# Performance work log

Hardware: AMD Instinct MI355X
Metric: run time of the kernel (lower is better)

## Reference

```python
import jax, jax.numpy as jnp
import numpy as np

# ---- constants from SystemsOfSprings.f ----
TS = 0.05                      # integration step h
K_G, C_G = 1.0, 2.0            # ground spring / damper (k1..k4, c1..c4)
K_I, C_I = 1.0, 0.0            # inter-agent spring / damper (k5..k10, c5..c10)
_L9 = float(np.sqrt(4.0 ** 2 + 1.5 ** 2))
EDGE_I = jnp.array([0, 1, 2, 3, 2, 3])          # springs 5,6,7,8,9,10
EDGE_J = jnp.array([1, 2, 3, 0, 0, 1])
EDGE_L = jnp.array([4.0, 1.5, 4.0, 1.5, _L9, _L9], dtype=jnp.float32)
XBAR = jnp.array([2.0, 2.0, 0.0, 0.0, -2.0, 2.0, 0.0, 0.0,
                  -2.0, -2.0, 0.0, 0.0, 2.0, -2.0, 0.0, 0.0], dtype=jnp.float32)


def _step(x, u, xbar):
    # x: (16,) = [px,py,vx,vy] x 4 agents; u: (8,) = 2 force inputs per agent
    px, py, vx, vy = x[0::4], x[1::4], x[2::4], x[3::4]      # (4,) each (Mx/My/Mvx/Mvy selections)
    xt, yt = xbar[0::4], xbar[1::4]

    # ground spring + damper forces (toward target, opposing velocity)
    dxt, dyt = px - xt, py - yt
    ang_t = jnp.arctan2(dyt, dxt)
    ang_v = jnp.arctan2(vy, vx)
    Fk0 = K_G * jnp.sqrt(dxt ** 2 + dyt ** 2)
    Fc0 = C_G * jnp.sqrt(vx ** 2 + vy ** 2)
    Fgx = -Fk0 * jnp.cos(ang_t) - Fc0 * jnp.cos(ang_v)
    Fgy = -Fk0 * jnp.sin(ang_t) - Fc0 * jnp.sin(ang_v)

    # inter-agent springs/dampers on the 6 edges (edge list, no 4x4 diagonal NaNs)
    dxe = px[EDGE_I] - px[EDGE_J]
    dye = py[EDGE_I] - py[EDGE_J]
    dvxe = vx[EDGE_I] - vx[EDGE_J]
    dvye = vy[EDGE_I] - vy[EDGE_J]
    Fke = K_I * (jnp.sqrt(dxe ** 2 + dye ** 2) - EDGE_L)
    Fce = C_I * jnp.sqrt(dvxe ** 2 + dvye ** 2)
    ang = jnp.arctan2(dye, dxe)      # angle from j toward i's perspective at i
    angv = jnp.arctan2(dvye, dvxe)
    cxe, sye = jnp.cos(ang), jnp.sin(ang)
    cve, sve = jnp.cos(angv), jnp.sin(angv)
    # force on agent i: -F*proj(i,j); on agent j: -F*proj(j,i) = +F*proj(i,j)
    z4 = jnp.zeros(4, x.dtype)
    Fsx = z4.at[EDGE_I].add(-Fke * cxe).at[EDGE_J].add(Fke * cxe)
    Fsy = z4.at[EDGE_I].add(-Fke * sye).at[EDGE_J].add(Fke * sye)
    Fdx = z4.at[EDGE_I].add(-Fce * cve).at[EDGE_J].add(Fce * cve)
    Fdy = z4.at[EDGE_I].add(-Fce * sve).at[EDGE_J].add(Fce * sve)

    accx = Fsx + Fdx + Fgx  # masses m1..m4 = 1
    accy = Fsy + Fdy + Fgy

    dx = jnp.zeros(16, x.dtype)
    dx = dx.at[0::4].set(vx).at[1::4].set(vy).at[2::4].set(accx).at[3::4].set(accy)
    Bu = jnp.zeros(16, x.dtype).at[2::4].set(u[0::2]).at[3::4].set(u[1::2])
    return x + (dx + Bu) * TS


def setup_inputs() -> dict:
    key = jax.random.key(0)
    kx, ku = jax.random.split(key)
    B = 1048576
    x = jax.random.normal(kx, (B, 16), dtype=jnp.float32)
    u = jax.random.normal(ku, (B, 8), dtype=jnp.float32)
    return {"t": 0, "x": x, "u": u, "w": jnp.zeros((16,), jnp.float32), "xbar": XBAR}


def reference(t, x, u, w, xbar):
    # t and w are unused, exactly as in the torch forward; batch via vmap
    return jax.vmap(lambda xi, ui: _step(xi, ui, xbar))(x, u)
```

## Files before the change

### kernel.cpp

```cpp
#include <hip/hip_runtime.h>
#include <math.h>


#define TS 0.05f

__global__ __launch_bounds__(256) void springs_node_kernel(
    const float* __restrict__ x,
    const float* __restrict__ u,
    float* __restrict__ out,
    int N)
{
    int g = blockIdx.x * blockDim.x + threadIdx.x;
    if (g >= N) return;

    int node = g & 3;

    float4 s  = reinterpret_cast<const float4*>(x)[g];
    float2 uc = reinterpret_cast<const float2*>(u)[g];

    float px = s.x, py = s.y, vx = s.z, vy = s.w;

    float xt = (node == 1 || node == 2) ? -2.f : 2.f;
    float yt = (node >= 2) ? -2.f : 2.f;

    float ax = -(px - xt) - 2.f * vx;
    float ay = -(py - yt) - 2.f * vy;

    const float Ld[3] = { 4.0f, 4.2720018727f , 1.5f };

#pragma unroll
    for (int d = 1; d <= 3; ++d) {
        float qx = __shfl_xor(px, d, 64);
        float qy = __shfl_xor(py, d, 64);
        float dx = px - qx;
        float dy = py - qy;
        float d2 = dx * dx + dy * dy;
        float L  = Ld[d - 1];

        float r    = sqrtf(d2);
        bool  nz   = (d2 > 0.f);
        float invr = nz ? (1.f / r) : 0.f;
        float c    = nz ? (dx * invr) : 1.f;
        float sn   = dy * invr;
        float Fk   = r - L;

        ax -= Fk * c;
        ay -= Fk * sn;
    }

    float4 r4;
    r4.x = px + TS * vx;
    r4.y = py + TS * vy;
    r4.z = vx + TS * (ax + uc.x);
    r4.w = vy + TS * (ay + uc.y);

    reinterpret_cast<float4*>(out)[g] = r4;
}

extern "C" void kernel_launch(void* const* d_in, const int* in_sizes, int n_in,
                              void* d_out, int out_size, void* d_ws, size_t ws_size,
                              hipStream_t stream) {
    const float* x = (const float*)d_in[1];
    const float* u = (const float*)d_in[2];
    float* out = (float*)d_out;

    int N = in_sizes[1] / 4;
    int block = 256;
    int grid = (N + block - 1) / block;
    springs_node_kernel<<<grid, block, 0, stream>>>(x, u, out, N);
}
```

Before: 147.0 us.

## Process two agent pairs per thread with DPP exchange and nontemporal stores

```diff
diff --git a/kernel.cpp b/kernel.cpp
--- a/kernel.cpp
+++ b/kernel.cpp
@@ -3,58 +3,107 @@
 
 
 #define TS 0.05f
+#define L9 4.2720018727f
 
-__global__ __launch_bounds__(256) void springs_node_kernel(
+typedef float f4v __attribute__((ext_vector_type(4)));
+
+__device__ __forceinline__ float dpp_xor1(float v) {
+    return __int_as_float(__builtin_amdgcn_update_dpp(
+        0, __float_as_int(v), 0xB1, 0xF, 0xF, true));
+}
+
+__device__ __forceinline__ void edge_acc(float dx, float dy, float L,
+                                         float& ax, float& ay) {
+    float d2   = dx * dx + dy * dy;
+    bool  nz   = d2 > 0.f;
+    float invr = nz ? rsqrtf(d2) : 0.f;
+    float r    = d2 * invr;
+    float c    = nz ? dx * invr : 1.f;
+    float sn   = dy * invr;
+    float Fk   = r - L;
+    ax -= Fk * c;
+    ay -= Fk * sn;
+}
+
+__device__ __forceinline__ void do_pair(int parity,
+                                        float4 a, float4 b, float4 uc,
+                                        float4& ra, float4& rb) {
+    float xtA = parity ? -2.f : 2.f;
+    float ytA = xtA;
+    float xtB = -xtA;
+    float ytB = ytA;
+
+    float axA = -(a.x - xtA) - 2.f * a.z;
+    float ayA = -(a.y - ytA) - 2.f * a.w;
+    float axB = -(b.x - xtB) - 2.f * b.z;
+    float ayB = -(b.y - ytB) - 2.f * b.w;
+
+    {
+        float dx = a.x - b.x, dy = a.y - b.y;
+        float d2   = dx * dx + dy * dy;
+        bool  nz   = d2 > 0.f;
+        float invr = nz ? rsqrtf(d2) : 0.f;
+        float r    = d2 * invr;
+        float c    = nz ? dx * invr : 1.f;
+        float sn   = dy * invr;
+        float Fk   = r - 4.0f;
+        float fx = Fk * c, fy = Fk * sn;
+        axA -= fx; ayA -= fy;
+        axB += fx; ayB += fy;
+    }
+
+    float pxA2 = dpp_xor1(a.x), pyA2 = dpp_xor1(a.y);
+    float pxB2 = dpp_xor1(b.x), pyB2 = dpp_xor1(b.y);
+
+    edge_acc(a.x - pxA2, a.y - pyA2, L9,   axA, ayA);
+    edge_acc(a.x - pxB2, a.y - pyB2, 1.5f, axA, ayA);
+    edge_acc(b.x - pxB2, b.y - pyB2, L9,   axB, ayB);
+    edge_acc(b.x - pxA2, b.y - pyA2, 1.5f, axB, ayB);
+
+    ra.x = a.x + TS * a.z;
+    ra.y = a.y + TS * a.w;
+    ra.z = a.z + TS * (axA + uc.x);
+    ra.w = a.w + TS * (ayA + uc.y);
+    rb.x = b.x + TS * b.z;
+    rb.y = b.y + TS * b.w;
+    rb.z = b.z + TS * (axB + uc.z);
+    rb.w = b.w + TS * (ayB + uc.w);
+}
+
+__device__ __forceinline__ void nt_store4(float4 v, float4* p) {
+    f4v t = { v.x, v.y, v.z, v.w };
+    __builtin_nontemporal_store(t, reinterpret_cast<f4v*>(p));
+}
+
+__global__ __launch_bounds__(256) void springs_pair2_kernel(
     const float* __restrict__ x,
     const float* __restrict__ u,
     float* __restrict__ out,
-    int N)
+    int T)
 {
     int g = blockIdx.x * blockDim.x + threadIdx.x;
-    if (g >= N) return;
+    if (g >= T) return;
+    int h = g + T;
 
-    int node = g & 3;
+    const float4* x4 = reinterpret_cast<const float4*>(x);
+    const float4* u4 = reinterpret_cast<const float4*>(u);
+    float4*       o4 = reinterpret_cast<float4*>(out);
 
-    float4 s  = reinterpret_cast<const float4*>(x)[g];
-    float2 uc = reinterpret_cast<const float2*>(u)[g];
+    float4 a0 = x4[2 * g];
+    float4 b0 = x4[2 * g + 1];
+    float4 a1 = x4[2 * h];
+    float4 b1 = x4[2 * h + 1];
+    float4 u0 = u4[g];
+    float4 u1 = u4[h];
 
-    float px = s.x, py = s.y, vx = s.z, vy = s.w;
+    float4 ra0, rb0, ra1, rb1;
+    do_pair(g & 1, a0, b0, u0, ra0, rb0);
+    do_pair(h & 1, a1, b1, u1, ra1, rb1);
 
-    float xt = (node == 1 || node == 2) ? -2.f : 2.f;
-    float yt = (node >= 2) ? -2.f : 2.f;
-
-    float ax = -(px - xt) - 2.f * vx;
-    float ay = -(py - yt) - 2.f * vy;
-
-    const float Ld[3] = { 4.0f, 4.2720018727f , 1.5f };
-
-#pragma unroll
-    for (int d = 1; d <= 3; ++d) {
-        float qx = __shfl_xor(px, d, 64);
-        float qy = __shfl_xor(py, d, 64);
-        float dx = px - qx;
-        float dy = py - qy;
-        float d2 = dx * dx + dy * dy;
-        float L  = Ld[d - 1];
-
-        float r    = sqrtf(d2);
-        bool  nz   = (d2 > 0.f);
-        float invr = nz ? (1.f / r) : 0.f;
-        float c    = nz ? (dx * invr) : 1.f;
-        float sn   = dy * invr;
-        float Fk   = r - L;
-
-        ax -= Fk * c;
-        ay -= Fk * sn;
-    }
-
-    float4 r4;
-    r4.x = px + TS * vx;
-    r4.y = py + TS * vy;
-    r4.z = vx + TS * (ax + uc.x);
-    r4.w = vy + TS * (ay + uc.y);
-
-    reinterpret_cast<float4*>(out)[g] = r4;
+    nt_store4(ra0, &o4[2 * g]);
+    nt_store4(rb0, &o4[2 * g + 1]);
+    nt_store4(ra1, &o4[2 * h]);
+    nt_store4(rb1, &o4[2 * h + 1]);
 }
 
 extern "C" void kernel_launch(void* const* d_in, const int* in_sizes, int n_in,
@@ -64,8 +113,8 @@
     const float* u = (const float*)d_in[2];
     float* out = (float*)d_out;
 
-    int N = in_sizes[1] / 4;
+    int T = in_sizes[1] / 16;
     int block = 256;
-    int grid = (N + block - 1) / block;
-    springs_node_kernel<<<grid, block, 0, stream>>>(x, u, out, N);
+    int grid = (T + block - 1) / block;
+    springs_pair2_kernel<<<grid, block, 0, stream>>>(x, u, out, T);
 }
```

Result: slower. 163.5 us (+11.2%).

## Process four strided node slices per thread and use DPP quad-permutes with rsqrt

Applied to the files above, without the earlier changes.

```diff
diff --git a/kernel.cpp b/kernel.cpp
--- a/kernel.cpp
+++ b/kernel.cpp
@@ -3,58 +3,78 @@
 
 
 #define TS 0.05f
+#define L9 4.2720018727f
 
-__global__ __launch_bounds__(256) void springs_node_kernel(
+template <int CTRL>
+__device__ __forceinline__ float dpp_qp(float v) {
+    return __int_as_float(__builtin_amdgcn_update_dpp(
+        0, __float_as_int(v), CTRL, 0xF, 0xF, true));
+}
+
+__device__ __forceinline__ void edge_acc(float dx, float dy, float L,
+                                         float& ax, float& ay) {
+    float d2   = dx * dx + dy * dy;
+    bool  nz   = d2 > 0.f;
+    float invr = nz ? rsqrtf(d2) : 0.f;
+    float r    = d2 * invr;
+    float c    = nz ? dx * invr : 1.f;
+    float sn   = dy * invr;
+    float Fk   = r - L;
+    ax -= Fk * c;
+    ay -= Fk * sn;
+}
+
+__device__ __forceinline__ float4 node_step(float4 s, float2 uc,
+                                            float xt, float yt) {
+    float ax = -(s.x - xt) - 2.f * s.z;
+    float ay = -(s.y - yt) - 2.f * s.w;
+
+    float qx1 = dpp_qp<0xB1>(s.x), qy1 = dpp_qp<0xB1>(s.y);
+    float qx2 = dpp_qp<0x4E>(s.x), qy2 = dpp_qp<0x4E>(s.y);
+    float qx3 = dpp_qp<0x1B>(s.x), qy3 = dpp_qp<0x1B>(s.y);
+
+    edge_acc(s.x - qx1, s.y - qy1, 4.0f, ax, ay);
+    edge_acc(s.x - qx2, s.y - qy2, L9,   ax, ay);
+    edge_acc(s.x - qx3, s.y - qy3, 1.5f, ax, ay);
+
+    float4 r;
+    r.x = s.x + TS * s.z;
+    r.y = s.y + TS * s.w;
+    r.z = s.z + TS * (ax + uc.x);
+    r.w = s.w + TS * (ay + uc.y);
+    return r;
+}
+
+__global__ __launch_bounds__(256) void springs_node4_kernel(
     const float* __restrict__ x,
     const float* __restrict__ u,
     float* __restrict__ out,
-    int N)
+    int S)
 {
     int g = blockIdx.x * blockDim.x + threadIdx.x;
-    if (g >= N) return;
+    if (g >= S) return;
+
+    const float4* x4 = reinterpret_cast<const float4*>(x);
+    const float2* u2 = reinterpret_cast<const float2*>(u);
+    float4*       o4 = reinterpret_cast<float4*>(out);
+
+    float4 s0 = x4[g];
+    float4 s1 = x4[g + S];
+    float4 s2 = x4[g + 2 * S];
+    float4 s3 = x4[g + 3 * S];
+    float2 c0 = u2[g];
+    float2 c1 = u2[g + S];
+    float2 c2 = u2[g + 2 * S];
+    float2 c3 = u2[g + 3 * S];
 
     int node = g & 3;
-
-    float4 s  = reinterpret_cast<const float4*>(x)[g];
-    float2 uc = reinterpret_cast<const float2*>(u)[g];
-
-    float px = s.x, py = s.y, vx = s.z, vy = s.w;
-
     float xt = (node == 1 || node == 2) ? -2.f : 2.f;
     float yt = (node >= 2) ? -2.f : 2.f;
 
-    float ax = -(px - xt) - 2.f * vx;
-    float ay = -(py - yt) - 2.f * vy;
-
-    const float Ld[3] = { 4.0f, 4.2720018727f , 1.5f };
-
-#pragma unroll
-    for (int d = 1; d <= 3; ++d) {
-        float qx = __shfl_xor(px, d, 64);
-        float qy = __shfl_xor(py, d, 64);
-        float dx = px - qx;
-        float dy = py - qy;
-        float d2 = dx * dx + dy * dy;
-        float L  = Ld[d - 1];
-
-        float r    = sqrtf(d2);
-        bool  nz   = (d2 > 0.f);
-        float invr = nz ? (1.f / r) : 0.f;
-        float c    = nz ? (dx * invr) : 1.f;
-        float sn   = dy * invr;
-        float Fk   = r - L;
-
-        ax -= Fk * c;
-        ay -= Fk * sn;
-    }
-
-    float4 r4;
-    r4.x = px + TS * vx;
-    r4.y = py + TS * vy;
-    r4.z = vx + TS * (ax + uc.x);
-    r4.w = vy + TS * (ay + uc.y);
-
-    reinterpret_cast<float4*>(out)[g] = r4;
+    o4[g]         = node_step(s0, c0, xt, yt);
+    o4[g + S]     = node_step(s1, c1, xt, yt);
+    o4[g + 2 * S] = node_step(s2, c2, xt, yt);
+    o4[g + 3 * S] = node_step(s3, c3, xt, yt);
 }
 
 extern "C" void kernel_launch(void* const* d_in, const int* in_sizes, int n_in,
@@ -65,7 +85,8 @@
     float* out = (float*)d_out;
 
     int N = in_sizes[1] / 4;
+    int S = N / 4;
     int block = 256;
-    int grid = (N + block - 1) / block;
-    springs_node_kernel<<<grid, block, 0, stream>>>(x, u, out, N);
+    int grid = (S + block - 1) / block;
+    springs_node4_kernel<<<grid, block, 0, stream>>>(x, u, out, S);
 }
```

Result: slower. 157.2 us (+7.0%).
